# Kernel optimization log

Measured on AMD Instinct MI355X. Metric: run time of the kernel, lower is better.

Reference implementation:

```python
import jax, jax.numpy as jnp
import numpy as np


def setup_inputs() -> dict:
    key = jax.random.key(0)
    k1, k2 = jax.random.split(key)
    x = jax.random.normal(k1, (16, 256, 128, 128), dtype=jnp.float32)
    # Conv2d(2, 1, 7, padding=3, bias=False) weight, OIHW layout
    conv_w = jax.random.normal(k2, (1, 2, 7, 7), dtype=jnp.float32) * 0.1
    return {"x": x, "conv_w": conv_w}


def reference(x, conv_w):
    # channel-wise mean and max pooling -> [B, 1, H, W] each
    avg_pool = jnp.mean(x, axis=1, keepdims=True)
    max_pool = jnp.max(x, axis=1, keepdims=True)
    cat = jnp.concatenate([avg_pool, max_pool], axis=1)  # [B, 2, H, W]
    # 7x7 conv, SAME padding (pad=3), NCHW / OIHW
    out = jax.lax.conv_general_dilated(
        cat, conv_w,
        window_strides=(1, 1),
        padding=((3, 3), (3, 3)),
        dimension_numbers=("NCHW", "OIHW", "NCHW"),
    )  # [B, 1, H, W]
    M = jax.nn.sigmoid(out)
    return x * M
```

## Files before the change

kernel.cpp:

```cpp
#include <hip/hip_runtime.h>
#include <math.h>

#define BB 16
#define CC 256
#define HH 128
#define WW 128
#define HWSZ (HH * WW)

typedef float floatx4 __attribute__((ext_vector_type(4)));

__global__ __launch_bounds__(256) void pool_kernel(const float* __restrict__ x,
                                                   float* __restrict__ avg_out,
                                                   float* __restrict__ max_out) {
    const int tf4   = threadIdx.x & 63;
    const int split = threadIdx.x >> 6;
    const int p0    = blockIdx.x * 256;
    const int b     = p0 >> 14;
    const int hw    = (p0 & (HWSZ - 1)) + tf4 * 4;

    const float* xb = x + (size_t)b * CC * HWSZ + hw;

    float4 s = make_float4(0.f, 0.f, 0.f, 0.f);
    float4 m = make_float4(-INFINITY, -INFINITY, -INFINITY, -INFINITY);

    const int c0 = split * 64;
    #pragma unroll 8
    for (int i = 0; i < 64; ++i) {
        float4 v = *(const float4*)(xb + (size_t)(c0 + i) * HWSZ);
        s.x += v.x; s.y += v.y; s.z += v.z; s.w += v.w;
        m.x = fmaxf(m.x, v.x); m.y = fmaxf(m.y, v.y);
        m.z = fmaxf(m.z, v.z); m.w = fmaxf(m.w, v.w);
    }

    __shared__ float4 sS[4][64];
    __shared__ float4 sM[4][64];
    sS[split][tf4] = s;
    sM[split][tf4] = m;
    __syncthreads();

    for (int off = 2; off >= 1; off >>= 1) {
        if (split < off) {
            float4 a  = sS[split][tf4], b2 = sS[split + off][tf4];
            a.x += b2.x; a.y += b2.y; a.z += b2.z; a.w += b2.w;
            sS[split][tf4] = a;
            float4 ma = sM[split][tf4], mb = sM[split + off][tf4];
            ma.x = fmaxf(ma.x, mb.x); ma.y = fmaxf(ma.y, mb.y);
            ma.z = fmaxf(ma.z, mb.z); ma.w = fmaxf(ma.w, mb.w);
            sM[split][tf4] = ma;
        }
        __syncthreads();
    }

    if (split == 0) {
        float4 a = sS[0][tf4];
        const float inv = 1.0f / CC;
        a.x *= inv; a.y *= inv; a.z *= inv; a.w *= inv;
        *(float4*)(avg_out + (size_t)b * HWSZ + hw) = a;
        *(float4*)(max_out + (size_t)b * HWSZ + hw) = sM[0][tf4];
    }
}

__global__ __launch_bounds__(256) void convmul_kernel(const float* __restrict__ x,
                                                      const float* __restrict__ avg_p,
                                                      const float* __restrict__ max_p,
                                                      const float* __restrict__ wgt,
                                                      float* __restrict__ out) {
    __shared__ float sw[98];
    __shared__ float sMl[256];

    const int tid = threadIdx.x;
    if (tid < 98) sw[tid] = wgt[tid];
    __syncthreads();

    const int strip = blockIdx.x;
    const int b     = strip >> 6;
    const int h0    = (strip & 63) * 2;

    {
        const int hl = tid >> 7;
        const int w  = tid & 127;
        const int h  = h0 + hl;
        const float* ap = avg_p + (size_t)b * HWSZ;
        const float* mp = max_p + (size_t)b * HWSZ;

        float acc = 0.f;
        #pragma unroll
        for (int kh = 0; kh < 7; ++kh) {
            const int hh = h + kh - 3;
            if (hh < 0 || hh >= HH) continue;
            #pragma unroll
            for (int kw = 0; kw < 7; ++kw) {
                const int ww2 = w + kw - 3;
                if (ww2 < 0 || ww2 >= WW) continue;
                const int off = hh * WW + ww2;
                acc += ap[off] * sw[kh * 7 + kw];
                acc += mp[off] * sw[49 + kh * 7 + kw];
            }
        }
        sMl[tid] = 1.0f / (1.0f + expf(-acc));
    }
    __syncthreads();

    const int g    = tid & 63;
    const int csub = tid >> 6;
    const floatx4 mv = ((const floatx4*)sMl)[g];

    const size_t base = (size_t)b * CC * HWSZ + (size_t)h0 * WW + (size_t)g * 4;
    const float* xp = x + base;
    float*       op = out + base;

    #pragma unroll 4
    for (int c = 0; c < 64; ++c) {
        const size_t coff = (size_t)(c * 4 + csub) * HWSZ;
        floatx4 xv = __builtin_nontemporal_load((const floatx4*)(xp + coff));
        __builtin_nontemporal_store(xv * mv, (floatx4*)(op + coff));
    }
}

extern "C" void kernel_launch(void* const* d_in, const int* in_sizes, int n_in,
                              void* d_out, int out_size, void* d_ws, size_t ws_size,
                              hipStream_t stream) {
    const float* x   = (const float*)d_in[0];
    const float* wgt = (const float*)d_in[1];
    float* out = (float*)d_out;

    float* avg_p = (float*)d_ws;
    float* max_p = avg_p + (size_t)BB * HWSZ;

    pool_kernel<<<1024, 256, 0, stream>>>(x, avg_p, max_p);

    convmul_kernel<<<1024, 256, 0, stream>>>(x, avg_p, max_p, wgt, out);
}
```

Before: 145.1 us.

## Split pipeline into partial pool, final pool, conv and reverse-order multiply kernels

Channel pooling is split into a partial pass over 16-channel groups and a small final reduction. The 7x7 conv plus sigmoid becomes its own kernel that writes a mask buffer. A grid-stride multiply kernel then walks x in reverse block order, so the most recently pooled part of x may still be in the last-level cache when it is read again. This adds extra workspace traffic for the partial sums and maxes, and it only runs when the workspace is large enough; otherwise the old two-kernel path is used.

```diff
diff --git a/kernel.cpp b/kernel.cpp
--- a/kernel.cpp
+++ b/kernel.cpp
@@ -8,6 +8,121 @@
 #define HWSZ (HH * WW)
 
 typedef float floatx4 __attribute__((ext_vector_type(4)));
+
+
+__global__ __launch_bounds__(256) void pool_partial_kernel(const float* __restrict__ x,
+                                                           float* __restrict__ psum,
+                                                           float* __restrict__ pmax) {
+    const int blk  = blockIdx.x;
+    const int b    = blk >> 5;
+    const int r    = blk & 31;
+    const int cg   = r >> 1;
+    const int half = r & 1;
+
+    const float* xb = x + (size_t)(b * CC + cg * 16) * HWSZ + half * (HWSZ / 2);
+    float* ps = psum + (size_t)(b * 16 + cg) * HWSZ + half * (HWSZ / 2);
+    float* pm = pmax + (size_t)(b * 16 + cg) * HWSZ + half * (HWSZ / 2);
+
+    for (int k = 0; k < 8; ++k) {
+        const int g4 = (k * 256 + threadIdx.x) * 4;
+        const float* p0 = xb + g4;
+
+        float4 s = make_float4(0.f, 0.f, 0.f, 0.f);
+        float4 m = make_float4(-INFINITY, -INFINITY, -INFINITY, -INFINITY);
+        #pragma unroll
+        for (int c = 0; c < 16; ++c) {
+            float4 v = *(const float4*)(p0 + (size_t)c * HWSZ);
+            s.x += v.x; s.y += v.y; s.z += v.z; s.w += v.w;
+            m.x = fmaxf(m.x, v.x); m.y = fmaxf(m.y, v.y);
+            m.z = fmaxf(m.z, v.z); m.w = fmaxf(m.w, v.w);
+        }
+        *(float4*)(ps + g4) = s;
+        *(float4*)(pm + g4) = m;
+    }
+}
+
+__global__ __launch_bounds__(256) void pool_final_kernel(const float* __restrict__ psum,
+                                                         const float* __restrict__ pmax,
+                                                         float* __restrict__ avg_out,
+                                                         float* __restrict__ max_out) {
+    const int i = blockIdx.x * 256 + threadIdx.x;
+    const int b = i >> 12;
+    const int g4 = (i & 4095) * 4;
+
+    const float* ps = psum + (size_t)b * 16 * HWSZ + g4;
+    const float* pm = pmax + (size_t)b * 16 * HWSZ + g4;
+
+    float4 s = make_float4(0.f, 0.f, 0.f, 0.f);
+    float4 m = make_float4(-INFINITY, -INFINITY, -INFINITY, -INFINITY);
+    #pragma unroll
+    for (int cg = 0; cg < 16; ++cg) {
+        float4 v = *(const float4*)(ps + (size_t)cg * HWSZ);
+        s.x += v.x; s.y += v.y; s.z += v.z; s.w += v.w;
+        float4 u = *(const float4*)(pm + (size_t)cg * HWSZ);
+        m.x = fmaxf(m.x, u.x); m.y = fmaxf(m.y, u.y);
+        m.z = fmaxf(m.z, u.z); m.w = fmaxf(m.w, u.w);
+    }
+    const float inv = 1.0f / CC;
+    s.x *= inv; s.y *= inv; s.z *= inv; s.w *= inv;
+    *(float4*)(avg_out + (size_t)b * HWSZ + g4) = s;
+    *(float4*)(max_out + (size_t)b * HWSZ + g4) = m;
+}
+
+__global__ __launch_bounds__(256) void conv_kernel(const float* __restrict__ avg_in,
+                                                   const float* __restrict__ max_in,
+                                                   const float* __restrict__ wgt,
+                                                   float* __restrict__ Mout) {
+    __shared__ float sw[98];
+    if (threadIdx.x < 98) sw[threadIdx.x] = wgt[threadIdx.x];
+    __syncthreads();
+
+    const int idx = blockIdx.x * blockDim.x + threadIdx.x;
+    const int b  = idx >> 14;
+    const int hw = idx & (HWSZ - 1);
+    const int h  = hw >> 7;
+    const int w  = hw & 127;
+
+    const float* ap = avg_in + (size_t)b * HWSZ;
+    const float* mp = max_in + (size_t)b * HWSZ;
+
+    float acc = 0.f;
+    #pragma unroll
+    for (int kh = 0; kh < 7; ++kh) {
+        const int hh = h + kh - 3;
+        if (hh < 0 || hh >= HH) continue;
+        #pragma unroll
+        for (int kw = 0; kw < 7; ++kw) {
+            const int ww2 = w + kw - 3;
+            if (ww2 < 0 || ww2 >= WW) continue;
+            const int off = hh * WW + ww2;
+            acc += ap[off] * sw[kh * 7 + kw];
+            acc += mp[off] * sw[49 + kh * 7 + kw];
+        }
+    }
+    Mout[idx] = 1.0f / (1.0f + expf(-acc));
+}
+
+__global__ __launch_bounds__(256) void mul_kernel(const float* __restrict__ x,
+                                                  const float* __restrict__ Mv,
+                                                  float* __restrict__ out) {
+    const int n4     = BB * CC * HWSZ / 4;
+    const int stride = gridDim.x * blockDim.x;
+    const int rbid   = gridDim.x - 1 - blockIdx.x;
+    const int base   = rbid * blockDim.x + threadIdx.x;
+    const int nIter  = n4 / stride;
+
+    const floatx4* xv4 = (const floatx4*)x;
+    floatx4*       ov4 = (floatx4*)out;
+
+    for (int it = nIter - 1; it >= 0; --it) {
+        const int i   = it * stride + base;
+        const int b   = i >> 20;
+        const int hw4 = i & 4095;
+        floatx4 xv = __builtin_nontemporal_load(xv4 + i);
+        floatx4 mv = *(const floatx4*)(Mv + ((size_t)b << 14) + (hw4 << 2));
+        __builtin_nontemporal_store(xv * mv, ov4 + i);
+    }
+}
 
 __global__ __launch_bounds__(256) void pool_kernel(const float* __restrict__ x,
                                                    float* __restrict__ avg_out,
@@ -124,10 +239,24 @@
     const float* wgt = (const float*)d_in[1];
     float* out = (float*)d_out;
 
-    float* avg_p = (float*)d_ws;
-    float* max_p = avg_p + (size_t)BB * HWSZ;
-
-    pool_kernel<<<1024, 256, 0, stream>>>(x, avg_p, max_p);
-
-    convmul_kernel<<<1024, 256, 0, stream>>>(x, avg_p, max_p, wgt, out);
-}
+    const size_t planeB = (size_t)BB * HWSZ;
+    const size_t need = (2 * 16 * planeB + 2 * planeB + planeB) * sizeof(float);
+
+    if (ws_size >= need) {
+        float* psum  = (float*)d_ws;
+        float* pmax  = psum + 16 * planeB;
+        float* avg_p = pmax + 16 * planeB;
+        float* max_p = avg_p + planeB;
+        float* Mbuf  = max_p + planeB;
+
+        pool_partial_kernel<<<512, 256, 0, stream>>>(x, psum, pmax);
+        pool_final_kernel<<<256, 256, 0, stream>>>(psum, pmax, avg_p, max_p);
+        conv_kernel<<<(BB * HWSZ) / 256, 256, 0, stream>>>(avg_p, max_p, wgt, Mbuf);
+        mul_kernel<<<4096, 256, 0, stream>>>(x, Mbuf, out);
+    } else {
+        float* avg_p = (float*)d_ws;
+        float* max_p = avg_p + planeB;
+        pool_kernel<<<1024, 256, 0, stream>>>(x, avg_p, max_p);
+        convmul_kernel<<<1024, 256, 0, stream>>>(x, avg_p, max_p, wgt, out);
+    }
+}
```

New measurement: 210.1 us. 44.8% more time.
